# Kernel tuning notes

Hardware: AMD Instinct MI355X
Metric: run time of the kernel (lower is better)

## Reference

```python
import jax, jax.numpy as jnp
import numpy as np

NUM_CLASSES = 24


def setup_inputs() -> dict:
    key = jax.random.key(0)
    k1, k2 = jax.random.split(key)
    data = jax.random.normal(k1, (8, 128, 128, 128), dtype=jnp.float32)
    label = jax.random.randint(k2, (8, 512, 512), 0, NUM_CLASSES, dtype=jnp.int64)
    return {"data": data, "label": label}


def reference(data, label):
    B, C, h, w = data.shape
    _, H, W = label.shape
    # nearest-neighbor interpolate to (H, W): torch 'nearest' uses floor(dst * src/dst)
    ri = (jnp.arange(H) * h) // H
    ci = (jnp.arange(W) * w) // W
    data_up = data[:, :, ri[:, None], ci[None, :]]  # [B, C, H, W]
    valid = label != -1                              # ignore mask
    lab = jnp.where(valid, label, 0)
    # scatter-add instead of one-hot + einsum (same math)
    seg = (lab + jnp.arange(B, dtype=lab.dtype)[:, None, None] * NUM_CLASSES).reshape(-1)
    x = (data_up * valid[:, None, :, :].astype(data.dtype))  # zero out ignored pixels
    x = x.transpose(0, 2, 3, 1).reshape(B * H * W, C)        # [B*H*W, C]
    sums = jax.ops.segment_sum(x, seg, num_segments=B * NUM_CLASSES)
    sums = sums.reshape(B, NUM_CLASSES, C)                   # [B, N, C]
    counts = jax.ops.segment_sum(valid.reshape(-1).astype(jnp.float32), seg,
                                 num_segments=B * NUM_CLASSES)
    counts = counts.reshape(B, NUM_CLASSES)                  # [B, N]
    feature = (sums / (counts[:, :, None] + 1e-8)).transpose(0, 2, 1)  # [B, C, N]
    mask = (counts > 0).astype(jnp.float32)                  # [B, N]
    return feature, mask
```

## Files before the change

### kernel.cpp

```cpp
#include <hip/hip_runtime.h>

#define NCLS 24
#define NB 8
#define NCH 128
#define WLO 128
#define WHI 512
#define CELLS (128*128)
#define SUBT 256
#define NBLK (NB * SUBT)
#define KCH (NCLS * NCH)
#define NF (NB * KCH)

typedef _Float16 f16x4 __attribute__((ext_vector_type(4)));
typedef _Float16 f16x8 __attribute__((ext_vector_type(8)));
typedef float    f32x4 __attribute__((ext_vector_type(4)));

#define HSWZ(c_, e_) ((e_) ^ (((c_) & 7) << 3))

__global__ __launch_bounds__(256, 4)
void fm_main(const float* __restrict__ data, const int* __restrict__ label,
             _Float16* __restrict__ part, float* __restrict__ cpart)
{
    __shared__ float    histf[32 * 64];
    __shared__ _Float16 tile[NCH * 64];

    const int bid  = blockIdx.x;
    const int b    = bid >> 8;
    const int grp  = bid & 255;
    const int tid  = threadIdx.x;

    const int q    = tid & 15;
    const int chb  = tid >> 4;
    const int r    = tid >> 6;
    const int cl   = tid & 63;
    const int w    = tid >> 6;
    const int lane = tid & 63;

    const int y  = grp >> 1;
    const int x0 = (grp & 1) << 6;
    const int cb = y * WLO + x0;

    const float* dbase = data  + (size_t)b * NCH * CELLS;
    const int*   lbase = label + (size_t)b * (WHI * WHI);

    float4 v[8];
#pragma unroll
    for (int k = 0; k < 8; ++k)
        v[k] = *reinterpret_cast<const float4*>(dbase + (size_t)(chb + k * 16) * CELLS + cb + q * 4);
    const int4 lv = *reinterpret_cast<const int4*>(lbase + (size_t)(4 * y + r) * WHI + x0 * 4 + cl * 4);

#pragma unroll
    for (int k = 0; k < 8; ++k) histf[tid + k * 256] = 0.f;
    __syncthreads();

    if ((unsigned)lv.x < 24u) atomicAdd(&histf[lv.x * 64 + HSWZ(lv.x, cl)], 1.f);
    if ((unsigned)lv.y < 24u) atomicAdd(&histf[lv.y * 64 + HSWZ(lv.y, cl)], 1.f);
    if ((unsigned)lv.z < 24u) atomicAdd(&histf[lv.z * 64 + HSWZ(lv.z, cl)], 1.f);
    if ((unsigned)lv.w < 24u) atomicAdd(&histf[lv.w * 64 + HSWZ(lv.w, cl)], 1.f);

#pragma unroll
    for (int k = 0; k < 8; ++k) {
        const int ch = chb + k * 16;
        f16x4 hv;
        hv[0] = (_Float16)v[k].x; hv[1] = (_Float16)v[k].y;
        hv[2] = (_Float16)v[k].z; hv[3] = (_Float16)v[k].w;
        const int idx = ch * 64 + ((((q >> 1) ^ (ch & 7)) << 3) | ((q & 1) << 2));
        *reinterpret_cast<f16x4*>(&tile[idx]) = hv;
    }
    __syncthreads();

    f16x8 af[2][2];
    float cs0 = 0.f, cs1 = 0.f;
#pragma unroll
    for (int mt = 0; mt < 2; ++mt)
#pragma unroll
        for (int kt = 0; kt < 2; ++kt) {
            const int cls = mt * 16 + (lane & 15);
            const int e0  = kt * 32 + (lane >> 4) * 8;
            const float* hp = &histf[cls * 64 + HSWZ(cls, e0)];
            const f32x4 h0 = *reinterpret_cast<const f32x4*>(hp);
            const f32x4 h1 = *reinterpret_cast<const f32x4*>(hp + 4);
            f16x8 a;
            a[0] = (_Float16)h0.x; a[1] = (_Float16)h0.y; a[2] = (_Float16)h0.z; a[3] = (_Float16)h0.w;
            a[4] = (_Float16)h1.x; a[5] = (_Float16)h1.y; a[6] = (_Float16)h1.z; a[7] = (_Float16)h1.w;
            af[mt][kt] = a;
            const float p = (h0.x + h0.y) + (h0.z + h0.w) + (h1.x + h1.y) + (h1.z + h1.w);
            if (mt == 0) cs0 += p; else cs1 += p;
        }

    f16x8 bf[2][2];
#pragma unroll
    for (int nt = 0; nt < 2; ++nt)
#pragma unroll
        for (int kt = 0; kt < 2; ++kt) {
            const int row = w * 32 + nt * 16 + (lane & 15);
            const int g   = kt * 4 + (lane >> 4);
            bf[nt][kt] = *reinterpret_cast<const f16x8*>(&tile[row * 64 + ((g ^ (row & 7)) << 3)]);
        }

    f32x4 acc[2][2];
#pragma unroll
    for (int mt = 0; mt < 2; ++mt)
#pragma unroll
        for (int nt = 0; nt < 2; ++nt) {
            acc[mt][nt] = (f32x4){0.f, 0.f, 0.f, 0.f};
#pragma unroll
            for (int kt = 0; kt < 2; ++kt)
                acc[mt][nt] = __builtin_amdgcn_mfma_f32_16x16x32_f16(
                    af[mt][kt], bf[nt][kt], acc[mt][nt], 0, 0, 0);
        }

    cs0 += __shfl_xor(cs0, 16, 64); cs0 += __shfl_xor(cs0, 32, 64);
    cs1 += __shfl_xor(cs1, 16, 64); cs1 += __shfl_xor(cs1, 32, 64);
    if (w == 0 && lane < 16) {
        cpart[(size_t)bid * NCLS + lane] = cs0;
        if (lane < 8) cpart[(size_t)bid * NCLS + 16 + lane] = cs1;
    }

    _Float16* pblk = part + (size_t)bid * KCH;
#pragma unroll
    for (int mt = 0; mt < 2; ++mt)
#pragma unroll
        for (int nt = 0; nt < 2; ++nt)
#pragma unroll
            for (int rg = 0; rg < 4; ++rg) {
                const int cls = mt * 16 + (lane >> 4) * 4 + rg;
                const int ch  = w * 32 + nt * 16 + (lane & 15);
                if (cls < NCLS) pblk[cls * NCH + ch] = (_Float16)acc[mt][nt][rg];
            }
}

__global__ __launch_bounds__(256)
void fm_final(const _Float16* __restrict__ part, const float* __restrict__ cpart,
              float* __restrict__ out)
{
    __shared__ float red[256];
    __shared__ float credv[256];
    const int bid  = blockIdx.x;
    const int b    = bid / (NCLS * 2);
    const int rem  = bid % (NCLS * 2);
    const int cls  = rem >> 1;
    const int half = rem & 1;
    const int t    = threadIdx.x;
    const int c    = t & 63;
    const int gq   = t >> 6;
    const int ch   = half * 64 + c;

    credv[t] = cpart[(size_t)(b * SUBT + t) * NCLS + cls];

    const _Float16* pb = part + (size_t)(b * SUBT + gq * 64) * KCH + cls * NCH + ch;
    float s = 0.f;
#pragma unroll 8
    for (int g = 0; g < 64; ++g) s += (float)pb[(size_t)g * KCH];
    red[t] = s;
    __syncthreads();

    if (t < 64) {
        float cnt = credv[t] + credv[t + 64] + credv[t + 128] + credv[t + 192];
#pragma unroll
        for (int o = 32; o >= 1; o >>= 1) cnt += __shfl_xor(cnt, o, 64);
        const float sf = red[t] + red[t + 64] + red[t + 128] + red[t + 192];
        out[(size_t)b * KCH + (half * 64 + t) * NCLS + cls] = sf / (cnt + 1e-8f);
        if (t == 0 && half == 0) out[NF + b * NCLS + cls] = (cnt > 0.f) ? 1.f : 0.f;
    }
}

extern "C" void kernel_launch(void* const* d_in, const int* in_sizes, int n_in,
                              void* d_out, int out_size, void* d_ws, size_t ws_size,
                              hipStream_t stream) {
    const float* data  = (const float*)d_in[0];
    const int*   label = (const int*)d_in[1];
    float*     out   = (float*)d_out;
    _Float16*  part  = (_Float16*)d_ws;
    float*     cpart = (float*)(part + (size_t)NBLK * KCH);

    fm_main<<<dim3(NBLK), dim3(256), 0, stream>>>(data, label, part, cpart);
    fm_final<<<dim3(NB * NCLS * 2), dim3(256), 0, stream>>>(part, cpart, out);
}
```

Measured before the change: 29.73 us.

## Process two sub-tiles per block with prefetch, halving partial buffers

Each block in the main kernel now handles a full low-res row (two 64-cell sub-tiles) in a loop, accumulating MFMA results in registers across both. Loads for the second sub-tile are issued before the barrier of the first, so they overlap the MFMA work. This halves the block count and the fp16 partial-sum traffic that the final reduction kernel reads. In exchange it adds extra barriers and serial work per block and lowers parallelism.

Measured after the change: 27.37 us. 1.09x faster.

```diff
diff --git a/kernel.cpp b/kernel.cpp
--- a/kernel.cpp
+++ b/kernel.cpp
@@ -6,8 +6,9 @@
 #define WLO 128
 #define WHI 512
 #define CELLS (128*128)
-#define SUBT 256
-#define NBLK (NB * SUBT)
+#define SUBS 2
+#define BPB 128
+#define NBLK (NB * BPB)
 #define KCH (NCLS * NCH)
 #define NF (NB * KCH)
 
@@ -25,8 +26,8 @@
     __shared__ _Float16 tile[NCH * 64];
 
     const int bid  = blockIdx.x;
-    const int b    = bid >> 8;
-    const int grp  = bid & 255;
+    const int b    = bid >> 7;
+    const int grp  = bid & 127;
     const int tid  = threadIdx.x;
 
     const int q    = tid & 15;
@@ -36,79 +37,95 @@
     const int w    = tid >> 6;
     const int lane = tid & 63;
 
-    const int y  = grp >> 1;
-    const int x0 = (grp & 1) << 6;
-    const int cb = y * WLO + x0;
-
     const float* dbase = data  + (size_t)b * NCH * CELLS;
-    const int*   lbase = label + (size_t)b * (WHI * WHI);
+    const int*   lbase = label + (size_t)b * (WHI * WHI) + (size_t)(4 * grp + r) * WHI;
 
     float4 v[8];
+    int4 lv;
+    {
+        const int cb = grp * WLO;
 #pragma unroll
-    for (int k = 0; k < 8; ++k)
-        v[k] = *reinterpret_cast<const float4*>(dbase + (size_t)(chb + k * 16) * CELLS + cb + q * 4);
-    const int4 lv = *reinterpret_cast<const int4*>(lbase + (size_t)(4 * y + r) * WHI + x0 * 4 + cl * 4);
-
-#pragma unroll
-    for (int k = 0; k < 8; ++k) histf[tid + k * 256] = 0.f;
-    __syncthreads();
-
-    if ((unsigned)lv.x < 24u) atomicAdd(&histf[lv.x * 64 + HSWZ(lv.x, cl)], 1.f);
-    if ((unsigned)lv.y < 24u) atomicAdd(&histf[lv.y * 64 + HSWZ(lv.y, cl)], 1.f);
-    if ((unsigned)lv.z < 24u) atomicAdd(&histf[lv.z * 64 + HSWZ(lv.z, cl)], 1.f);
-    if ((unsigned)lv.w < 24u) atomicAdd(&histf[lv.w * 64 + HSWZ(lv.w, cl)], 1.f);
-
-#pragma unroll
-    for (int k = 0; k < 8; ++k) {
-        const int ch = chb + k * 16;
-        f16x4 hv;
-        hv[0] = (_Float16)v[k].x; hv[1] = (_Float16)v[k].y;
-        hv[2] = (_Float16)v[k].z; hv[3] = (_Float16)v[k].w;
-        const int idx = ch * 64 + ((((q >> 1) ^ (ch & 7)) << 3) | ((q & 1) << 2));
-        *reinterpret_cast<f16x4*>(&tile[idx]) = hv;
+        for (int k = 0; k < 8; ++k)
+            v[k] = *reinterpret_cast<const float4*>(dbase + (size_t)(chb + k * 16) * CELLS + cb + q * 4);
+        lv = *reinterpret_cast<const int4*>(lbase + cl * 4);
     }
-    __syncthreads();
-
-    f16x8 af[2][2];
-    float cs0 = 0.f, cs1 = 0.f;
-#pragma unroll
-    for (int mt = 0; mt < 2; ++mt)
-#pragma unroll
-        for (int kt = 0; kt < 2; ++kt) {
-            const int cls = mt * 16 + (lane & 15);
-            const int e0  = kt * 32 + (lane >> 4) * 8;
-            const float* hp = &histf[cls * 64 + HSWZ(cls, e0)];
-            const f32x4 h0 = *reinterpret_cast<const f32x4*>(hp);
-            const f32x4 h1 = *reinterpret_cast<const f32x4*>(hp + 4);
-            f16x8 a;
-            a[0] = (_Float16)h0.x; a[1] = (_Float16)h0.y; a[2] = (_Float16)h0.z; a[3] = (_Float16)h0.w;
-            a[4] = (_Float16)h1.x; a[5] = (_Float16)h1.y; a[6] = (_Float16)h1.z; a[7] = (_Float16)h1.w;
-            af[mt][kt] = a;
-            const float p = (h0.x + h0.y) + (h0.z + h0.w) + (h1.x + h1.y) + (h1.z + h1.w);
-            if (mt == 0) cs0 += p; else cs1 += p;
-        }
-
-    f16x8 bf[2][2];
-#pragma unroll
-    for (int nt = 0; nt < 2; ++nt)
-#pragma unroll
-        for (int kt = 0; kt < 2; ++kt) {
-            const int row = w * 32 + nt * 16 + (lane & 15);
-            const int g   = kt * 4 + (lane >> 4);
-            bf[nt][kt] = *reinterpret_cast<const f16x8*>(&tile[row * 64 + ((g ^ (row & 7)) << 3)]);
-        }
 
     f32x4 acc[2][2];
 #pragma unroll
     for (int mt = 0; mt < 2; ++mt)
 #pragma unroll
-        for (int nt = 0; nt < 2; ++nt) {
-            acc[mt][nt] = (f32x4){0.f, 0.f, 0.f, 0.f};
+        for (int nt = 0; nt < 2; ++nt) acc[mt][nt] = (f32x4){0.f, 0.f, 0.f, 0.f};
+    float cs0 = 0.f, cs1 = 0.f;
+
 #pragma unroll
-            for (int kt = 0; kt < 2; ++kt)
-                acc[mt][nt] = __builtin_amdgcn_mfma_f32_16x16x32_f16(
-                    af[mt][kt], bf[nt][kt], acc[mt][nt], 0, 0, 0);
+    for (int s = 0; s < SUBS; ++s) {
+#pragma unroll
+        for (int k = 0; k < 8; ++k) histf[tid + k * 256] = 0.f;
+        __syncthreads();
+
+        if ((unsigned)lv.x < 24u) atomicAdd(&histf[lv.x * 64 + HSWZ(lv.x, cl)], 1.f);
+        if ((unsigned)lv.y < 24u) atomicAdd(&histf[lv.y * 64 + HSWZ(lv.y, cl)], 1.f);
+        if ((unsigned)lv.z < 24u) atomicAdd(&histf[lv.z * 64 + HSWZ(lv.z, cl)], 1.f);
+        if ((unsigned)lv.w < 24u) atomicAdd(&histf[lv.w * 64 + HSWZ(lv.w, cl)], 1.f);
+
+#pragma unroll
+        for (int k = 0; k < 8; ++k) {
+            const int ch = chb + k * 16;
+            f16x4 hv;
+            hv[0] = (_Float16)v[k].x; hv[1] = (_Float16)v[k].y;
+            hv[2] = (_Float16)v[k].z; hv[3] = (_Float16)v[k].w;
+            const int idx = ch * 64 + ((((q >> 1) ^ (ch & 7)) << 3) | ((q & 1) << 2));
+            *reinterpret_cast<f16x4*>(&tile[idx]) = hv;
         }
+
+        if (s + 1 < SUBS) {
+            const int cb = grp * WLO + 64;
+#pragma unroll
+            for (int k = 0; k < 8; ++k)
+                v[k] = *reinterpret_cast<const float4*>(dbase + (size_t)(chb + k * 16) * CELLS + cb + q * 4);
+            lv = *reinterpret_cast<const int4*>(lbase + 256 + cl * 4);
+        }
+        __syncthreads();
+
+        f16x8 af[2][2];
+#pragma unroll
+        for (int mt = 0; mt < 2; ++mt)
+#pragma unroll
+            for (int kt = 0; kt < 2; ++kt) {
+                const int cls = mt * 16 + (lane & 15);
+                const int e0  = kt * 32 + (lane >> 4) * 8;
+                const float* hp = &histf[cls * 64 + HSWZ(cls, e0)];
+                const f32x4 h0 = *reinterpret_cast<const f32x4*>(hp);
+                const f32x4 h1 = *reinterpret_cast<const f32x4*>(hp + 4);
+                f16x8 a;
+                a[0] = (_Float16)h0.x; a[1] = (_Float16)h0.y; a[2] = (_Float16)h0.z; a[3] = (_Float16)h0.w;
+                a[4] = (_Float16)h1.x; a[5] = (_Float16)h1.y; a[6] = (_Float16)h1.z; a[7] = (_Float16)h1.w;
+                af[mt][kt] = a;
+                const float p = (h0.x + h0.y) + (h0.z + h0.w) + (h1.x + h1.y) + (h1.z + h1.w);
+                if (mt == 0) cs0 += p; else cs1 += p;
+            }
+
+        f16x8 bf[2][2];
+#pragma unroll
+        for (int nt = 0; nt < 2; ++nt)
+#pragma unroll
+            for (int kt = 0; kt < 2; ++kt) {
+                const int row = w * 32 + nt * 16 + (lane & 15);
+                const int g   = kt * 4 + (lane >> 4);
+                bf[nt][kt] = *reinterpret_cast<const f16x8*>(&tile[row * 64 + ((g ^ (row & 7)) << 3)]);
+            }
+
+#pragma unroll
+        for (int mt = 0; mt < 2; ++mt)
+#pragma unroll
+            for (int nt = 0; nt < 2; ++nt)
+#pragma unroll
+                for (int kt = 0; kt < 2; ++kt)
+                    acc[mt][nt] = __builtin_amdgcn_mfma_f32_16x16x32_f16(
+                        af[mt][kt], bf[nt][kt], acc[mt][nt], 0, 0, 0);
+
+        if (s + 1 < SUBS) __syncthreads();
+    }
 
     cs0 += __shfl_xor(cs0, 16, 64); cs0 += __shfl_xor(cs0, 32, 64);
     cs1 += __shfl_xor(cs1, 16, 64); cs1 += __shfl_xor(cs1, 32, 64);
@@ -135,7 +152,7 @@
               float* __restrict__ out)
 {
     __shared__ float red[256];
-    __shared__ float credv[256];
+    __shared__ float credv[128];
     const int bid  = blockIdx.x;
     const int b    = bid / (NCLS * 2);
     const int rem  = bid % (NCLS * 2);
@@ -144,19 +161,18 @@
     const int t    = threadIdx.x;
     const int c    = t & 63;
     const int gq   = t >> 6;
-    const int ch   = half * 64 + c;
 
-    credv[t] = cpart[(size_t)(b * SUBT + t) * NCLS + cls];
+    if (t < 128) credv[t] = cpart[(size_t)(b * BPB + t) * NCLS + cls];
 
-    const _Float16* pb = part + (size_t)(b * SUBT + gq * 64) * KCH + cls * NCH + ch;
+    const _Float16* pb = part + (size_t)(b * BPB + gq * 32) * KCH + cls * NCH + half * 64 + c;
     float s = 0.f;
 #pragma unroll 8
-    for (int g = 0; g < 64; ++g) s += (float)pb[(size_t)g * KCH];
+    for (int g = 0; g < 32; ++g) s += (float)pb[(size_t)g * KCH];
     red[t] = s;
     __syncthreads();
 
     if (t < 64) {
-        float cnt = credv[t] + credv[t + 64] + credv[t + 128] + credv[t + 192];
+        float cnt = credv[t] + credv[t + 64];
 #pragma unroll
         for (int o = 32; o >= 1; o >>= 1) cnt += __shfl_xor(cnt, o, 64);
         const float sf = red[t] + red[t + 64] + red[t + 128] + red[t + 192];
```

## Load data tile directly into LDS and overlap with histogram build

Applied to the files above, without the earlier changes.

Replaces register-staged loads plus fp16 conversion and LDS store with asynchronous global_load_lds into an fp32 LDS tile, so each wave loads its own 32-channel rows. The histogram build runs under barriers that skip the vector memory drain, with a vmcnt wait placed only before the tile is read. The fp32-to-fp16 conversion moves to the B-fragment read. Swizzles are dropped, so LDS bank conflicts on the tile and histogram reads become possible, and the fp32 tile doubles LDS use, which may reduce occupancy.

Measured after the change: 36.49 us. +22.7%, slower.

```diff
diff --git a/kernel.cpp b/kernel.cpp
--- a/kernel.cpp
+++ b/kernel.cpp
@@ -11,63 +11,61 @@
 #define KCH (NCLS * NCH)
 #define NF (NB * KCH)
 
-typedef _Float16 f16x4 __attribute__((ext_vector_type(4)));
 typedef _Float16 f16x8 __attribute__((ext_vector_type(8)));
 typedef float    f32x4 __attribute__((ext_vector_type(4)));
 
-#define HSWZ(c_, e_) ((e_) ^ (((c_) & 7) << 3))
+__device__ __forceinline__ void barrier_nodrain() {
+    asm volatile("s_waitcnt lgkmcnt(0)" ::: "memory");
+    __builtin_amdgcn_s_barrier();
+}
+
+__device__ __forceinline__ void load_lds16(const float* g, float* l) {
+    __builtin_amdgcn_global_load_lds(
+        (const __attribute__((address_space(1))) void*)g,
+        (__attribute__((address_space(3))) void*)l, 16, 0, 0);
+}
 
 __global__ __launch_bounds__(256, 4)
 void fm_main(const float* __restrict__ data, const int* __restrict__ label,
              _Float16* __restrict__ part, float* __restrict__ cpart)
 {
-    __shared__ float    histf[32 * 64];
-    __shared__ _Float16 tile[NCH * 64];
+    __shared__ float tile[NCH * 64];
+    __shared__ float histf[32 * 64];
 
     const int bid  = blockIdx.x;
     const int b    = bid >> 8;
     const int grp  = bid & 255;
     const int tid  = threadIdx.x;
 
-    const int q    = tid & 15;
-    const int chb  = tid >> 4;
-    const int r    = tid >> 6;
-    const int cl   = tid & 63;
     const int w    = tid >> 6;
     const int lane = tid & 63;
+    const int cl   = lane;
+    const int wb   = w * 32;
 
     const int y  = grp >> 1;
     const int x0 = (grp & 1) << 6;
     const int cb = y * WLO + x0;
 
-    const float* dbase = data  + (size_t)b * NCH * CELLS;
-    const int*   lbase = label + (size_t)b * (WHI * WHI);
+    const float* dbase = data + (size_t)b * NCH * CELLS + cb + (lane & 15) * 4;
+    const int*   lbase = label + (size_t)b * (WHI * WHI) + (size_t)(4 * y + w) * WHI + x0 * 4;
 
-    float4 v[8];
+    const int4 lv = *reinterpret_cast<const int4*>(lbase + cl * 4);
+    __builtin_amdgcn_sched_barrier(0);
+
 #pragma unroll
     for (int k = 0; k < 8; ++k)
-        v[k] = *reinterpret_cast<const float4*>(dbase + (size_t)(chb + k * 16) * CELLS + cb + q * 4);
-    const int4 lv = *reinterpret_cast<const int4*>(lbase + (size_t)(4 * y + r) * WHI + x0 * 4 + cl * 4);
+        load_lds16(dbase + (size_t)(wb + k * 4 + (lane >> 4)) * CELLS,
+                   &tile[(wb + k * 4) * 64]);
 
-#pragma unroll
-    for (int k = 0; k < 8; ++k) histf[tid + k * 256] = 0.f;
-    __syncthreads();
+    reinterpret_cast<f32x4*>(histf)[tid]       = (f32x4){0.f, 0.f, 0.f, 0.f};
+    reinterpret_cast<f32x4*>(histf)[tid + 256] = (f32x4){0.f, 0.f, 0.f, 0.f};
+    barrier_nodrain();
 
-    if ((unsigned)lv.x < 24u) atomicAdd(&histf[lv.x * 64 + HSWZ(lv.x, cl)], 1.f);
-    if ((unsigned)lv.y < 24u) atomicAdd(&histf[lv.y * 64 + HSWZ(lv.y, cl)], 1.f);
-    if ((unsigned)lv.z < 24u) atomicAdd(&histf[lv.z * 64 + HSWZ(lv.z, cl)], 1.f);
-    if ((unsigned)lv.w < 24u) atomicAdd(&histf[lv.w * 64 + HSWZ(lv.w, cl)], 1.f);
-
-#pragma unroll
-    for (int k = 0; k < 8; ++k) {
-        const int ch = chb + k * 16;
-        f16x4 hv;
-        hv[0] = (_Float16)v[k].x; hv[1] = (_Float16)v[k].y;
-        hv[2] = (_Float16)v[k].z; hv[3] = (_Float16)v[k].w;
-        const int idx = ch * 64 + ((((q >> 1) ^ (ch & 7)) << 3) | ((q & 1) << 2));
-        *reinterpret_cast<f16x4*>(&tile[idx]) = hv;
-    }
-    __syncthreads();
+    if ((unsigned)lv.x < 24u) atomicAdd(&histf[lv.x * 64 + cl], 1.f);
+    if ((unsigned)lv.y < 24u) atomicAdd(&histf[lv.y * 64 + cl], 1.f);
+    if ((unsigned)lv.z < 24u) atomicAdd(&histf[lv.z * 64 + cl], 1.f);
+    if ((unsigned)lv.w < 24u) atomicAdd(&histf[lv.w * 64 + cl], 1.f);
+    barrier_nodrain();
 
     f16x8 af[2][2];
     float cs0 = 0.f, cs1 = 0.f;
@@ -77,7 +75,7 @@
         for (int kt = 0; kt < 2; ++kt) {
             const int cls = mt * 16 + (lane & 15);
             const int e0  = kt * 32 + (lane >> 4) * 8;
-            const float* hp = &histf[cls * 64 + HSWZ(cls, e0)];
+            const float* hp = &histf[cls * 64 + e0];
             const f32x4 h0 = *reinterpret_cast<const f32x4*>(hp);
             const f32x4 h1 = *reinterpret_cast<const f32x4*>(hp + 4);
             f16x8 a;
@@ -88,14 +86,21 @@
             if (mt == 0) cs0 += p; else cs1 += p;
         }
 
+    asm volatile("s_waitcnt vmcnt(0)" ::: "memory");
+
     f16x8 bf[2][2];
 #pragma unroll
     for (int nt = 0; nt < 2; ++nt)
 #pragma unroll
         for (int kt = 0; kt < 2; ++kt) {
-            const int row = w * 32 + nt * 16 + (lane & 15);
-            const int g   = kt * 4 + (lane >> 4);
-            bf[nt][kt] = *reinterpret_cast<const f16x8*>(&tile[row * 64 + ((g ^ (row & 7)) << 3)]);
+            const int row = wb + nt * 16 + (lane & 15);
+            const float* tp = &tile[row * 64 + kt * 32 + (lane >> 4) * 8];
+            const f32x4 b0 = *reinterpret_cast<const f32x4*>(tp);
+            const f32x4 b1 = *reinterpret_cast<const f32x4*>(tp + 4);
+            f16x8 v;
+            v[0] = (_Float16)b0.x; v[1] = (_Float16)b0.y; v[2] = (_Float16)b0.z; v[3] = (_Float16)b0.w;
+            v[4] = (_Float16)b1.x; v[5] = (_Float16)b1.y; v[6] = (_Float16)b1.z; v[7] = (_Float16)b1.w;
+            bf[nt][kt] = v;
         }
 
     f32x4 acc[2][2];
@@ -125,7 +130,7 @@
 #pragma unroll
             for (int rg = 0; rg < 4; ++rg) {
                 const int cls = mt * 16 + (lane >> 4) * 4 + rg;
-                const int ch  = w * 32 + nt * 16 + (lane & 15);
+                const int ch  = wb + nt * 16 + (lane & 15);
                 if (cls < NCLS) pblk[cls * NCH + ch] = (_Float16)acc[mt][nt][rg];
             }
 }
@@ -144,11 +149,10 @@
     const int t    = threadIdx.x;
     const int c    = t & 63;
     const int gq   = t >> 6;
-    const int ch   = half * 64 + c;
 
     credv[t] = cpart[(size_t)(b * SUBT + t) * NCLS + cls];
 
-    const _Float16* pb = part + (size_t)(b * SUBT + gq * 64) * KCH + cls * NCH + ch;
+    const _Float16* pb = part + (size_t)(b * SUBT + gq * 64) * KCH + cls * NCH + half * 64 + c;
     float s = 0.f;
 #pragma unroll 8
     for (int g = 0; g < 64; ++g) s += (float)pb[(size_t)g * KCH];
```
